# Kernel optimization log

Hardware: AMD Instinct MI355X
Metric: run time of the kernel (lower is better)

The kernel has to match this reference:

```python
import jax, jax.numpy as jnp
import numpy as np

NEG_BIG = -9e15

def setup_inputs() -> dict:
    key = jax.random.key(0)
    k1, k2, k3, k4 = jax.random.split(key, 4)
    N, Fin, Fout = 8192, 128, 64
    x = jax.random.normal(k1, (N, Fin), dtype=jnp.float32)
    adj = jax.random.randint(k2, (N, N), 0, 2).astype(jnp.float32)
    W = jax.random.normal(k3, (Fin, Fout), dtype=jnp.float32) * (1.0 / np.sqrt(Fin))
    a = jax.random.normal(k4, (2 * Fout, 1), dtype=jnp.float32) * (1.0 / np.sqrt(2 * Fout))
    return {"x": x, "adj": adj, "W": W, "a": a}

def reference(x, adj, W, a):
    Fout = W.shape[1]
    Wh = x @ W                              # [N, Fout]
    Wh1 = Wh @ a[:Fout, :]                  # [N, 1]
    Wh2 = Wh @ a[Fout:, :]                  # [N, 1]
    e = jax.nn.leaky_relu(Wh1 + Wh2.T, negative_slope=0.2)  # [N, N]
    attention = jnp.where(adj > 0, e, NEG_BIG)
    attention = jax.nn.softmax(attention, axis=1)
    # dropout is identity in eval mode (training=False)
    h_prime = attention @ Wh                # [N, Fout]
    return jax.nn.elu(h_prime)
```

## Files before the change

### kernel.cpp

```cpp
#include <hip/hip_runtime.h>
#include <cstdint>
#include <cstddef>


#define NN   8192
#define FIN  128
#define FOUT 64
#define SJ   8
#define JCHUNK (NN / SJ)

typedef __attribute__((ext_vector_type(8))) short   short8;
typedef __attribute__((ext_vector_type(4))) float   f32x4;

__global__ __launch_bounds__(256) void gat_phaseA(
    const float* __restrict__ x, const float* __restrict__ W,
    const float* __restrict__ a, unsigned short* __restrict__ Whbt,
    float* __restrict__ Wh1, float* __restrict__ Wh2)
{
  const int wid  = threadIdx.x >> 6;
  const int lane = threadIdx.x & 63;
  const int row  = blockIdx.x * 4 + wid;
  const float* xr = x + row * FIN;
  const float a1 = a[lane];
  const float a2 = a[FOUT + lane];
  float acc = 0.f;
#pragma unroll 8
  for (int k = 0; k < FIN; ++k)
    acc = fmaf(xr[k], W[k * FOUT + lane], acc);
  unsigned int u = __float_as_uint(acc);
  unsigned int r = (u + 0x7FFFu + ((u >> 16) & 1u)) >> 16;
  Whbt[lane * NN + row] = (unsigned short)r;
  float s1 = acc * a1, s2 = acc * a2;
#pragma unroll
  for (int off = 32; off; off >>= 1) {
    s1 += __shfl_xor(s1, off);
    s2 += __shfl_xor(s2, off);
  }
  if (lane == 0) { Wh1[row] = s1; Wh2[row] = s2; }
}

__global__ __launch_bounds__(256, 4) void gat_phaseB(
    const float* __restrict__ adj, const unsigned short* __restrict__ Whbt,
    const float* __restrict__ Wh1, const float* __restrict__ Wh2,
    float* __restrict__ accbuf, float* __restrict__ denbuf, int nslices)
{
  const int wid  = threadIdx.x >> 6;
  const int lane = threadIdx.x & 63;
  const int task = blockIdx.x * 4 + wid;
  const int rowTile = task / SJ;
  const int jc      = task % SJ;
  const int m = lane & 15;
  const int q = lane >> 4;
  const int row = rowTile * 16 + m;
  const float wh1 = Wh1[row];
  const float* adjrow = adj + (size_t)row * NN;
  const unsigned short* bbase = Whbt + m * NN;

  f32x4 c0 = {0.f,0.f,0.f,0.f}, c1 = c0, c2 = c0, c3 = c0;
  float rsum = 0.f;

  const int jbeg = jc * JCHUNK;
  for (int jb = jbeg; jb < jbeg + JCHUNK; jb += 32) {
    const int j0 = jb + q * 8;
    f32x4 ad0 = __builtin_nontemporal_load((const f32x4*)(adjrow + j0));
    f32x4 ad1 = __builtin_nontemporal_load((const f32x4*)(adjrow + j0 + 4));
    f32x4 w20 = *(const f32x4*)(Wh2 + j0);
    f32x4 w21 = *(const f32x4*)(Wh2 + j0 + 4);
    short8 af;
#pragma unroll
    for (int e = 0; e < 4; ++e) {
      {
        float t = wh1 + w20[e];
        t = fmaxf(t, 0.2f * t);
        float p = __expf(t);
        p = (ad0[e] > 0.f) ? p : 0.f;
        unsigned int pu = __float_as_uint(p) & 0xFFFF0000u;
        rsum += __uint_as_float(pu);
        af[e] = (short)(pu >> 16);
      }
      {
        float t = wh1 + w21[e];
        t = fmaxf(t, 0.2f * t);
        float p = __expf(t);
        p = (ad1[e] > 0.f) ? p : 0.f;
        unsigned int pu = __float_as_uint(p) & 0xFFFF0000u;
        rsum += __uint_as_float(pu);
        af[4 + e] = (short)(pu >> 16);
      }
    }
    const unsigned short* bp = bbase + j0;
    c0 = __builtin_amdgcn_mfma_f32_16x16x32_bf16(af, *(const short8*)(bp          ), c0, 0, 0, 0);
    c1 = __builtin_amdgcn_mfma_f32_16x16x32_bf16(af, *(const short8*)(bp + 16 * NN), c1, 0, 0, 0);
    c2 = __builtin_amdgcn_mfma_f32_16x16x32_bf16(af, *(const short8*)(bp + 32 * NN), c2, 0, 0, 0);
    c3 = __builtin_amdgcn_mfma_f32_16x16x32_bf16(af, *(const short8*)(bp + 48 * NN), c3, 0, 0, 0);
  }

  rsum += __shfl_xor(rsum, 16);
  rsum += __shfl_xor(rsum, 32);

  const int slice = (nslices > 1) ? jc : 0;
  float* accout = accbuf + (size_t)slice * (NN * FOUT);
  float* denout = denbuf + slice * NN;
  f32x4 cc[4] = {c0, c1, c2, c3};
  if (nslices > 1) {
    if (q == 0) denout[row] = rsum;
#pragma unroll
    for (int ft = 0; ft < 4; ++ft)
#pragma unroll
      for (int r = 0; r < 4; ++r)
        accout[(rowTile * 16 + q * 4 + r) * FOUT + ft * 16 + m] = cc[ft][r];
  } else {
    if (q == 0) atomicAdd(&denout[row], rsum);
#pragma unroll
    for (int ft = 0; ft < 4; ++ft)
#pragma unroll
      for (int r = 0; r < 4; ++r)
        atomicAdd(&accout[(rowTile * 16 + q * 4 + r) * FOUT + ft * 16 + m], cc[ft][r]);
  }
}

__global__ __launch_bounds__(256) void gat_phaseC(
    const float* __restrict__ accbuf, const float* __restrict__ denbuf,
    float* __restrict__ out, int nslices)
{
  const int idx = blockIdx.x * 256 + threadIdx.x;
  const int row = idx >> 6;
  float s = 0.f, d = 0.f;
  for (int sl = 0; sl < nslices; ++sl) {
    s += accbuf[(size_t)sl * (NN * FOUT) + idx];
    d += denbuf[sl * NN + row];
  }
  float v = s / d;
  out[idx] = (v > 0.f) ? v : expm1f(v);
}

extern "C" void kernel_launch(void* const* d_in, const int* in_sizes, int n_in,
                              void* d_out, int out_size, void* d_ws, size_t ws_size,
                              hipStream_t stream)
{
  const float* x   = (const float*)d_in[0];
  const float* adj = (const float*)d_in[1];
  const float* W   = (const float*)d_in[2];
  const float* a   = (const float*)d_in[3];
  float* out = (float*)d_out;

  const size_t accEl = (size_t)NN * FOUT;
  const size_t roomyBytes = SJ * accEl * 4 + (size_t)SJ * NN * 4
                          + (size_t)NN * 8 + (size_t)FOUT * NN * 2;
  const int nslices = (ws_size >= roomyBytes) ? SJ : 1;

  char* ws = (char*)d_ws;
  float* accbuf = (float*)ws;
  size_t off = (size_t)nslices * accEl * 4;
  float* denbuf = (float*)(ws + off); off += (size_t)nslices * NN * 4;
  float* Wh1 = (float*)(ws + off);    off += (size_t)NN * 4;
  float* Wh2 = (float*)(ws + off);    off += (size_t)NN * 4;
  unsigned short* Whbt = (unsigned short*)(ws + off);

  if (nslices == 1)
    hipMemsetAsync(accbuf, 0, accEl * 4 + (size_t)NN * 4, stream);

  gat_phaseA<<<NN / 4, 256, 0, stream>>>(x, W, a, Whbt, Wh1, Wh2);
  gat_phaseB<<<(512 * SJ) / 4, 256, 0, stream>>>(adj, Whbt, Wh1, Wh2,
                                                 accbuf, denbuf, nslices);
  gat_phaseC<<<(NN * FOUT) / 256, 256, 0, stream>>>(accbuf, denbuf, out, nslices);
}
```

Baseline: 448.2 us.

## Prefetch adjacency rows, multiply by mask, vectorize phase A and C

Phase B now software-prefetches the next adjacency chunk one iteration ahead, so the dominant streaming load of adj overlaps with the exp and MFMA work. The select on adj>0 becomes a multiply, which relies on adj holding only 0/1 values. Phase A uses float4 loads of x with four independent accumulators, and phase C processes four outputs per thread with vector loads and a reciprocal. Register pressure rises in phase B, and the multiply-by-adj assumption only holds for binary adjacency matrices.

```diff
diff --git a/kernel.cpp b/kernel.cpp
--- a/kernel.cpp
+++ b/kernel.cpp
@@ -23,10 +23,16 @@
   const float* xr = x + row * FIN;
   const float a1 = a[lane];
   const float a2 = a[FOUT + lane];
-  float acc = 0.f;
+  float acc0 = 0.f, acc1 = 0.f, acc2 = 0.f, acc3 = 0.f;
 #pragma unroll 8
-  for (int k = 0; k < FIN; ++k)
-    acc = fmaf(xr[k], W[k * FOUT + lane], acc);
+  for (int k = 0; k < FIN; k += 4) {
+    float4 xv = *(const float4*)(xr + k);
+    acc0 = fmaf(xv.x, W[(k + 0) * FOUT + lane], acc0);
+    acc1 = fmaf(xv.y, W[(k + 1) * FOUT + lane], acc1);
+    acc2 = fmaf(xv.z, W[(k + 2) * FOUT + lane], acc2);
+    acc3 = fmaf(xv.w, W[(k + 3) * FOUT + lane], acc3);
+  }
+  float acc = (acc0 + acc1) + (acc2 + acc3);
   unsigned int u = __float_as_uint(acc);
   unsigned int r = (u + 0x7FFFu + ((u >> 16) & 1u)) >> 16;
   Whbt[lane * NN + row] = (unsigned short)r;
@@ -60,10 +66,16 @@
   float rsum = 0.f;
 
   const int jbeg = jc * JCHUNK;
-  for (int jb = jbeg; jb < jbeg + JCHUNK; jb += 32) {
+  const int jend = jbeg + JCHUNK;
+  f32x4 ad0 = __builtin_nontemporal_load((const f32x4*)(adjrow + jbeg + q * 8));
+  f32x4 ad1 = __builtin_nontemporal_load((const f32x4*)(adjrow + jbeg + q * 8 + 4));
+
+  for (int jb = jbeg; jb < jend; jb += 32) {
     const int j0 = jb + q * 8;
-    f32x4 ad0 = __builtin_nontemporal_load((const f32x4*)(adjrow + j0));
-    f32x4 ad1 = __builtin_nontemporal_load((const f32x4*)(adjrow + j0 + 4));
+    const int jn = (jb + 32 < jend) ? (j0 + 32) : (jbeg + q * 8);
+    f32x4 nd0 = __builtin_nontemporal_load((const f32x4*)(adjrow + jn));
+    f32x4 nd1 = __builtin_nontemporal_load((const f32x4*)(adjrow + jn + 4));
+
     f32x4 w20 = *(const f32x4*)(Wh2 + j0);
     f32x4 w21 = *(const f32x4*)(Wh2 + j0 + 4);
     short8 af;
@@ -72,8 +84,7 @@
       {
         float t = wh1 + w20[e];
         t = fmaxf(t, 0.2f * t);
-        float p = __expf(t);
-        p = (ad0[e] > 0.f) ? p : 0.f;
+        float p = __expf(t) * ad0[e];
         unsigned int pu = __float_as_uint(p) & 0xFFFF0000u;
         rsum += __uint_as_float(pu);
         af[e] = (short)(pu >> 16);
@@ -81,8 +92,7 @@
       {
         float t = wh1 + w21[e];
         t = fmaxf(t, 0.2f * t);
-        float p = __expf(t);
-        p = (ad1[e] > 0.f) ? p : 0.f;
+        float p = __expf(t) * ad1[e];
         unsigned int pu = __float_as_uint(p) & 0xFFFF0000u;
         rsum += __uint_as_float(pu);
         af[4 + e] = (short)(pu >> 16);
@@ -93,6 +103,8 @@
     c1 = __builtin_amdgcn_mfma_f32_16x16x32_bf16(af, *(const short8*)(bp + 16 * NN), c1, 0, 0, 0);
     c2 = __builtin_amdgcn_mfma_f32_16x16x32_bf16(af, *(const short8*)(bp + 32 * NN), c2, 0, 0, 0);
     c3 = __builtin_amdgcn_mfma_f32_16x16x32_bf16(af, *(const short8*)(bp + 48 * NN), c3, 0, 0, 0);
+
+    ad0 = nd0; ad1 = nd1;
   }
 
   rsum += __shfl_xor(rsum, 16);
@@ -123,15 +135,24 @@
     const float* __restrict__ accbuf, const float* __restrict__ denbuf,
     float* __restrict__ out, int nslices)
 {
-  const int idx = blockIdx.x * 256 + threadIdx.x;
-  const int row = idx >> 6;
-  float s = 0.f, d = 0.f;
+  const int idx4 = blockIdx.x * 256 + threadIdx.x;
+  const int idx  = idx4 * 4;
+  const int row  = idx >> 6;
+  f32x4 s = {0.f, 0.f, 0.f, 0.f};
+  float d = 0.f;
   for (int sl = 0; sl < nslices; ++sl) {
-    s += accbuf[(size_t)sl * (NN * FOUT) + idx];
+    f32x4 v = *(const f32x4*)(accbuf + (size_t)sl * (NN * FOUT) + idx);
+    s += v;
     d += denbuf[sl * NN + row];
   }
-  float v = s / d;
-  out[idx] = (v > 0.f) ? v : expm1f(v);
+  float inv = 1.0f / d;
+  f32x4 o;
+#pragma unroll
+  for (int e = 0; e < 4; ++e) {
+    float v = s[e] * inv;
+    o[e] = (v > 0.f) ? v : expm1f(v);
+  }
+  *(f32x4*)(out + idx) = o;
 }
 
 extern "C" void kernel_launch(void* const* d_in, const int* in_sizes, int n_in,
@@ -163,5 +184,5 @@
   gat_phaseA<<<NN / 4, 256, 0, stream>>>(x, W, a, Whbt, Wh1, Wh2);
   gat_phaseB<<<(512 * SJ) / 4, 256, 0, stream>>>(adj, Whbt, Wh1, Wh2,
                                                  accbuf, denbuf, nslices);
-  gat_phaseC<<<(NN * FOUT) / 256, 256, 0, stream>>>(accbuf, denbuf, out, nslices);
+  gat_phaseC<<<(NN * FOUT) / 4 / 256, 256, 0, stream>>>(accbuf, denbuf, out, nslices);
 }
```

Result: no change. 442.6 us (-1.3%).
